# Kernel tuning notes

Measured on AMD Instinct MI355X. Metric: run time of the kernel, lower is better.

The kernel has to match this reference:

```python
import jax, jax.numpy as jnp
import numpy as np

EPS = 1.1920928955078125e-07  # torch fp32 default eps for F.rms_norm
N_HEADS = 16
HEAD_DIM = 128


def apply_rotary_emb(x, cos, sin):
    # x: [B,S,H,D]; cos/sin: [1,S,1,D/2]
    d = x.shape[-1] // 2
    x1, x2 = x[..., :d], x[..., d:]
    return jnp.concatenate([x1 * cos + x2 * sin, -x1 * sin + x2 * cos], axis=-1)


def rms_norm(x):
    # F.rms_norm over last dim, no learned weight
    ms = jnp.mean(jnp.square(x), axis=-1, keepdims=True)
    return x * jax.lax.rsqrt(ms + EPS)


def setup_inputs() -> dict:
    key = jax.random.key(0)
    ks = jax.random.split(key, 7)
    B, S, D = 2, 2048, 2048
    half = HEAD_DIM // 2
    # rotary tables (built like standard RoPE for realism)
    inv_freq = 1.0 / (10000.0 ** (np.arange(0, half, dtype=np.float32) / half))
    t = np.arange(S, dtype=np.float32)
    freqs = np.outer(t, inv_freq)  # [S, D/2]
    cos = jnp.asarray(np.cos(freqs))[None, :, None, :]
    sin = jnp.asarray(np.sin(freqs))[None, :, None, :]
    sd = 1.0 / np.sqrt(D)
    return {
        "x": jax.random.normal(ks[0], (B, S, D), jnp.float32),
        "cos": cos,
        "sin": sin,
        "Wq": jax.random.normal(ks[1], (D, D), jnp.float32) * sd,
        "Wk": jax.random.normal(ks[2], (D, D), jnp.float32) * sd,
        "Wv": jax.random.normal(ks[3], (D, D), jnp.float32) * sd,
        "Wo": jax.random.normal(ks[4], (D, D), jnp.float32) * sd,
    }


def reference(x, cos, sin, Wq, Wk, Wv, Wo):
    B, S, D = x.shape
    H, Hd = N_HEADS, HEAD_DIM
    q = (x @ Wq.T).reshape(B, S, H, Hd)
    k = (x @ Wk.T).reshape(B, S, H, Hd)
    v = (x @ Wv.T).reshape(B, S, H, Hd)
    q = apply_rotary_emb(q, cos[:, :S], sin[:, :S])
    k = apply_rotary_emb(k, cos[:, :S], sin[:, :S])
    q = rms_norm(q) * 1.2  # [B,S,H,Hd]
    k = rms_norm(k) * 1.2
    scale = 1.0 / jnp.sqrt(jnp.asarray(Hd, x.dtype))
    # scores: [B,H,Sq,Sk]
    scores = jnp.einsum("bqhd,bkhd->bhqk", q, k) * scale
    attn = jax.nn.softmax(scores, axis=-1)
    y = jnp.einsum("bhqk,bkhd->bqhd", attn, v).reshape(B, S, D)
    return y @ Wo.T
```

## Files before the change

### kernel.cpp

```cpp
#include <hip/hip_runtime.h>
#include <hip/hip_bf16.h>
#include <math.h>

typedef __bf16 bf16;
typedef __attribute__((ext_vector_type(8))) __bf16 bf16x8;
typedef __attribute__((ext_vector_type(4))) float f32x4;
typedef __attribute__((ext_vector_type(16))) float f32x16;

#define DEV __device__ __forceinline__

DEV void gload16(const void* g, void* l) {
    __builtin_amdgcn_global_load_lds(
        (__attribute__((address_space(1))) void*)(void*)g,
        (__attribute__((address_space(3))) void*)l, 16, 0, 0);
}

DEV unsigned pk2(float a, float b) {
    union { bf16 h[2]; unsigned u; } z;
    z.h[0] = (bf16)a; z.h[1] = (bf16)b;
    return z.u;
}

DEV void plswap(unsigned& a, unsigned& b) {
    asm volatile("v_permlane32_swap_b32 %0, %1" : "+v"(a), "+v"(b));
}

__global__ __launch_bounds__(256) void cvt_kernel(const float* __restrict__ in,
                                                  bf16* __restrict__ out, int n8) {
    for (int i = blockIdx.x * 256 + threadIdx.x; i < n8; i += gridDim.x * 256) {
        const float4* p = (const float4*)(in + (size_t)i * 8);
        float4 a = p[0], b = p[1];
        bf16x8 o;
        o[0] = (bf16)a.x; o[1] = (bf16)a.y; o[2] = (bf16)a.z; o[3] = (bf16)a.w;
        o[4] = (bf16)b.x; o[5] = (bf16)b.y; o[6] = (bf16)b.z; o[7] = (bf16)b.w;
        *(bf16x8*)(out + (size_t)i * 8) = o;
    }
}

template <bool F32OUT>
__global__ __launch_bounds__(256) void gemm_bt(const bf16* __restrict__ A,
                                               const bf16* __restrict__ B,
                                               void* __restrict__ Cout,
                                               int M, int N, int K) {
    __shared__ __align__(16) bf16 As[128 * 64];
    __shared__ __align__(16) bf16 Bs[128 * 64];
    const int tid = threadIdx.x, lane = tid & 63, wv = tid >> 6;
    const int tm = blockIdx.y * 128, tn = blockIdx.x * 128;
    const int wr = (wv >> 1) * 64, wc = (wv & 1) * 64;

    f32x4 acc[4][4] = {};
    const int scb = (lane & 7) * 16;

    for (int k0 = 0; k0 < K; k0 += 64) {
#pragma unroll
        for (int i = 0; i < 4; ++i) {
            int chunk = wv * 4 + i;
            int row = chunk * 8 + (lane >> 3);
            int cb = scb ^ ((row & 7) << 4);
            gload16((const char*)(A + (size_t)(tm + row) * K + k0) + cb,
                    (char*)As + chunk * 1024);
            gload16((const char*)(B + (size_t)(tn + row) * K + k0) + cb,
                    (char*)Bs + chunk * 1024);
        }
        __syncthreads();
#pragma unroll
        for (int kk = 0; kk < 2; ++kk) {
            bf16x8 af[4], bfr[4];
#pragma unroll
            for (int m = 0; m < 4; ++m) {
                int row = wr + m * 16 + (lane & 15);
                int cb = (kk * 64 + ((lane >> 4) * 16)) ^ ((row & 7) << 4);
                af[m] = *(const bf16x8*)((const char*)As + row * 128 + cb);
            }
#pragma unroll
            for (int n = 0; n < 4; ++n) {
                int row = wc + n * 16 + (lane & 15);
                int cb = (kk * 64 + ((lane >> 4) * 16)) ^ ((row & 7) << 4);
                bfr[n] = *(const bf16x8*)((const char*)Bs + row * 128 + cb);
            }
#pragma unroll
            for (int m = 0; m < 4; ++m)
#pragma unroll
                for (int n = 0; n < 4; ++n)
                    acc[m][n] = __builtin_amdgcn_mfma_f32_16x16x32_bf16(
                        af[m], bfr[n], acc[m][n], 0, 0, 0);
        }
        __syncthreads();
    }
#pragma unroll
    for (int m = 0; m < 4; ++m)
#pragma unroll
        for (int n = 0; n < 4; ++n)
#pragma unroll
            for (int r = 0; r < 4; ++r) {
                int row = tm + wr + m * 16 + (lane >> 4) * 4 + r;
                int col = tn + wc + n * 16 + (lane & 15);
                if (F32OUT)
                    ((float*)Cout)[(size_t)row * N + col] = acc[m][n][r];
                else
                    ((bf16*)Cout)[(size_t)row * N + col] = (bf16)acc[m][n][r];
            }
}

__global__ __launch_bounds__(256) void rope_rms(bf16* __restrict__ q,
                                                bf16* __restrict__ k,
                                                const float* __restrict__ cosp,
                                                const float* __restrict__ sinp) {
    int gw = blockIdx.x * 4 + (threadIdx.x >> 6);
    int lane = threadIdx.x & 63;
    bf16* base = (blockIdx.y == 0) ? q : k;
    int m = gw >> 4, h = gw & 15;
    int s = m & 2047;
    bf16* p = base + (size_t)m * 2048 + h * 128;
    float x1 = (float)p[lane], x2 = (float)p[lane + 64];
    float c = cosp[s * 64 + lane], si = sinp[s * 64 + lane];
    float r1 = x1 * c + x2 * si;
    float r2 = x2 * c - x1 * si;
    float ss = r1 * r1 + r2 * r2;
#pragma unroll
    for (int msk = 1; msk < 64; msk <<= 1) ss += __shfl_xor(ss, msk);
    float sc = rsqrtf(ss * (1.0f / 128.0f) + 1.1920928955078125e-07f) * 1.2f;
    if (blockIdx.y == 0) sc *= (0.08838834764831845f * 1.4426950408889634f);
    p[lane] = (bf16)(r1 * sc);
    p[lane + 64] = (bf16)(r2 * sc);
}

__global__ __launch_bounds__(256, 2) void attn_kernel(const bf16* __restrict__ q,
                                                      const bf16* __restrict__ k,
                                                      const bf16* __restrict__ v,
                                                      bf16* __restrict__ y) {
    __shared__ __align__(16) bf16 Ks[2][64 * 128];
    __shared__ __align__(16) bf16 Vt[2][128][72];

    const int tid = threadIdx.x, lane = tid & 63, wv = tid >> 6;
    const int q31 = lane & 31, h5 = lane >> 5;

    int wgid = blockIdx.y * 16 + blockIdx.x;
    int xcd = wgid & 7, j = wgid >> 3;
    int bh = xcd * 4 + (j >> 4);
    int qblk = j & 15;
    const int b = bh >> 4, h = bh & 15;
    const int q0 = qblk * 128;

    const bf16* qptr = q + (size_t)(b * 2048 + q0 + wv * 32 + q31) * 2048 +
                       h * 128 + h5 * 8;
    bf16x8 qf[8];
#pragma unroll
    for (int ks = 0; ks < 8; ++ks) qf[ks] = *(const bf16x8*)(qptr + ks * 16);

    float mrun = -INFINITY, lrun = 0.f;
    f32x16 acco[4] = {};

    const bf16* vbase = v + (size_t)(b * 2048 + wv * 16) * 2048 + h * 128 + 2 * lane;
    const bf16* kbase = k + (size_t)(b * 2048) * 2048 + h * 128;

    unsigned u[16];

    auto stageK = [&](int t, int buf) {
#pragma unroll
        for (int i = 0; i < 4; ++i) {
            int chunk = wv * 4 + i;
            int row = chunk * 4 + (lane >> 4);
            int cb = ((lane & 15) * 16) ^ ((row & 7) << 4);
            gload16((const char*)(kbase + (size_t)(t * 64 + row) * 2048) + cb,
                    (char*)(Ks[buf]) + chunk * 1024);
        }
    };
    auto loadV = [&](int t) {
        const bf16* vp = vbase + (size_t)(t * 64) * 2048;
#pragma unroll
        for (int jj = 0; jj < 16; ++jj)
            u[jj] = *(const unsigned*)(vp + (size_t)jj * 2048);
    };
    auto writeV = [&](int buf) {
        union { unsigned short s[8]; bf16x8 v8; } r0a, r0b, r1a, r1b;
#pragma unroll
        for (int jj = 0; jj < 8; ++jj) {
            r0a.s[jj] = (unsigned short)(u[jj] & 0xffff);
            r1a.s[jj] = (unsigned short)(u[jj] >> 16);
            r0b.s[jj] = (unsigned short)(u[jj + 8] & 0xffff);
            r1b.s[jj] = (unsigned short)(u[jj + 8] >> 16);
        }
        *(bf16x8*)(&Vt[buf][2 * lane][wv * 16]) = r0a.v8;
        *(bf16x8*)(&Vt[buf][2 * lane][wv * 16 + 8]) = r0b.v8;
        *(bf16x8*)(&Vt[buf][2 * lane + 1][wv * 16]) = r1a.v8;
        *(bf16x8*)(&Vt[buf][2 * lane + 1][wv * 16 + 8]) = r1b.v8;
    };

    stageK(0, 0);
    loadV(0);
    writeV(0);
    __syncthreads();

    for (int t = 0; t < 32; ++t) {
        const int c = t & 1;
        if (t < 31) {
            stageK(t + 1, c ^ 1);
            loadV(t + 1);
        }

        f32x16 st[2];
        __builtin_amdgcn_s_setprio(1);
#pragma unroll
        for (int kvb = 0; kvb < 2; ++kvb) {
            f32x16 a = {};
#pragma unroll
            for (int ks = 0; ks < 8; ++ks) {
                int row = kvb * 32 + q31;
                int cb = (32 * ks + 16 * h5) ^ ((row & 7) << 4);
                const bf16x8 kf =
                    *(const bf16x8*)((const char*)(Ks[c]) + row * 256 + cb);
                a = __builtin_amdgcn_mfma_f32_32x32x16_bf16(kf, qf[ks], a, 0, 0, 0);
            }
            st[kvb] = a;
        }
        __builtin_amdgcn_s_setprio(0);

        float t8[8];
#pragma unroll
        for (int r = 0; r < 8; ++r)
            t8[r] = fmaxf(fmaxf(st[0][r], st[0][r + 8]),
                          fmaxf(st[1][r], st[1][r + 8]));
        float mx = fmaxf(fmaxf(fmaxf(t8[0], t8[1]), fmaxf(t8[2], t8[3])),
                         fmaxf(fmaxf(t8[4], t8[5]), fmaxf(t8[6], t8[7])));
        mx = fmaxf(mx, __shfl_xor(mx, 32));

        if (__any(mx - mrun > 8.0f)) {
            float mn = fmaxf(mrun, mx);
            float alpha = exp2f(mrun - mn);
            mrun = mn;
            lrun *= alpha;
#pragma unroll
            for (int r = 0; r < 16; ++r) {
                int qr = (r & 3) + 8 * (r >> 2) + 4 * h5;
                float al = __shfl(alpha, qr);
                acco[0][r] *= al; acco[1][r] *= al;
                acco[2][r] *= al; acco[3][r] *= al;
            }
        }

        unsigned w[2][8];
        float rsa = 0.f, rsb = 0.f;
#pragma unroll
        for (int kvb = 0; kvb < 2; ++kvb)
#pragma unroll
            for (int i = 0; i < 8; ++i) {
                float p0 = exp2f(st[kvb][2 * i] - mrun);
                float p1 = exp2f(st[kvb][2 * i + 1] - mrun);
                if (i & 1) rsb += p0 + p1; else rsa += p0 + p1;
                w[kvb][i] = pk2(p0, p1);
            }
        float rs = rsa + rsb;
        rs += __shfl_xor(rs, 32);
        lrun += rs;

        __builtin_amdgcn_s_setprio(1);
#pragma unroll
        for (int b2 = 0; b2 < 2; ++b2)
#pragma unroll
            for (int ksl = 0; ksl < 2; ++ksl) {
                const int ks = b2 * 2 + ksl, u0 = ksl * 4;
                unsigned f0 = w[b2][u0 + 0], f2 = w[b2][u0 + 2];
                unsigned f1 = w[b2][u0 + 1], f3 = w[b2][u0 + 3];
                plswap(f0, f2);
                plswap(f1, f3);
                union { unsigned uu[4]; bf16x8 v8; } fr;
                fr.uu[0] = f0; fr.uu[1] = f1; fr.uu[2] = f2; fr.uu[3] = f3;
#pragma unroll
                for (int dblk = 0; dblk < 4; ++dblk) {
                    const bf16x8 vf = *(const bf16x8*)(
                        &Vt[c][dblk * 32 + q31][ks * 16 + h5 * 8]);
                    acco[dblk] = __builtin_amdgcn_mfma_f32_32x32x16_bf16(
                        fr.v8, vf, acco[dblk], 0, 0, 0);
                }
            }
        __builtin_amdgcn_s_setprio(0);

        if (t < 31) writeV(c ^ 1);
        __syncthreads();
    }

    float linv = 1.0f / lrun;
#pragma unroll
    for (int r = 0; r < 16; ++r) {
        int qr = (r & 3) + 8 * (r >> 2) + 4 * h5;
        float il = __shfl(linv, qr);
        size_t row = (size_t)(b * 2048 + q0 + wv * 32 + qr) * 2048 + h * 128;
#pragma unroll
        for (int dblk = 0; dblk < 4; ++dblk)
            y[row + dblk * 32 + q31] = (bf16)(acco[dblk][r] * il);
    }
}

extern "C" void kernel_launch(void* const* d_in, const int* in_sizes, int n_in,
                              void* d_out, int out_size, void* d_ws, size_t ws_size,
                              hipStream_t stream) {
    const float* x = (const float*)d_in[0];
    const float* cs = (const float*)d_in[1];
    const float* sn = (const float*)d_in[2];
    const float* Wq = (const float*)d_in[3];
    const float* Wk = (const float*)d_in[4];
    const float* Wv = (const float*)d_in[5];
    const float* Wo = (const float*)d_in[6];

    char* ws = (char*)d_ws;
    bf16* xb  = (bf16*)(ws + 0);
    bf16* wqb = (bf16*)(ws + 16777216);
    bf16* wkb = (bf16*)(ws + 25165824);
    bf16* wvb = (bf16*)(ws + 33554432);
    bf16* wob = (bf16*)(ws + 41943040);
    bf16* qb  = (bf16*)(ws + 50331648);
    bf16* kb  = (bf16*)(ws + 67108864);
    bf16* vb  = (bf16*)(ws + 83886080);
    bf16* yb  = (bf16*)(ws + 100663296);

    cvt_kernel<<<1024, 256, 0, stream>>>(x, xb, 8388608 / 8);
    cvt_kernel<<<512, 256, 0, stream>>>(Wq, wqb, 4194304 / 8);
    cvt_kernel<<<512, 256, 0, stream>>>(Wk, wkb, 4194304 / 8);
    cvt_kernel<<<512, 256, 0, stream>>>(Wv, wvb, 4194304 / 8);
    cvt_kernel<<<512, 256, 0, stream>>>(Wo, wob, 4194304 / 8);

    dim3 g(16, 32);
    gemm_bt<false><<<g, 256, 0, stream>>>(xb, wqb, qb, 4096, 2048, 2048);
    gemm_bt<false><<<g, 256, 0, stream>>>(xb, wkb, kb, 4096, 2048, 2048);
    gemm_bt<false><<<g, 256, 0, stream>>>(xb, wvb, vb, 4096, 2048, 2048);

    rope_rms<<<dim3(16384, 2), 256, 0, stream>>>(qb, kb, cs, sn);

    attn_kernel<<<dim3(16, 32), 256, 0, stream>>>(qb, kb, vb, yb);

    gemm_bt<true><<<g, 256, 0, stream>>>(yb, wob, d_out, 4096, 2048, 2048);
}
```

Measured before the change: 326.7 us.

## Double per-wave query rows in attention and merge weight conversion launches

Each attention wave now handles two 32-row query sub-tiles (256 queries per block), so every K and V fragment read from LDS feeds two MFMAs. This halves the grid to 256 blocks and lowers occupancy to one block per CU. The four weight fp32-to-bf16 conversions become a single launch. The changes aim to cut LDS traffic and K/V reloads per query and to save launch overhead, at the cost of higher register pressure and fewer resident waves to hide latency.

```diff
diff --git a/kernel.cpp b/kernel.cpp
--- a/kernel.cpp
+++ b/kernel.cpp
@@ -34,6 +34,24 @@
         o[0] = (bf16)a.x; o[1] = (bf16)a.y; o[2] = (bf16)a.z; o[3] = (bf16)a.w;
         o[4] = (bf16)b.x; o[5] = (bf16)b.y; o[6] = (bf16)b.z; o[7] = (bf16)b.w;
         *(bf16x8*)(out + (size_t)i * 8) = o;
+    }
+}
+
+__global__ __launch_bounds__(256) void cvtw_kernel(const float* __restrict__ w0,
+                                                   const float* __restrict__ w1,
+                                                   const float* __restrict__ w2,
+                                                   const float* __restrict__ w3,
+                                                   bf16* __restrict__ out) {
+    const float* in = (blockIdx.y == 0) ? w0 : (blockIdx.y == 1) ? w1
+                      : (blockIdx.y == 2) ? w2 : w3;
+    bf16* o = out + (size_t)blockIdx.y * 4194304;
+    for (int i = blockIdx.x * 256 + threadIdx.x; i < 524288; i += 512 * 256) {
+        const float4* p = (const float4*)(in + (size_t)i * 8);
+        float4 a = p[0], b = p[1];
+        bf16x8 v;
+        v[0] = (bf16)a.x; v[1] = (bf16)a.y; v[2] = (bf16)a.z; v[3] = (bf16)a.w;
+        v[4] = (bf16)b.x; v[5] = (bf16)b.y; v[6] = (bf16)b.z; v[7] = (bf16)b.w;
+        *(bf16x8*)(o + (size_t)i * 8) = v;
     }
 }
 
@@ -125,7 +143,7 @@
     p[lane + 64] = (bf16)(r2 * sc);
 }
 
-__global__ __launch_bounds__(256, 2) void attn_kernel(const bf16* __restrict__ q,
+__global__ __launch_bounds__(256, 1) void attn_kernel(const bf16* __restrict__ q,
                                                       const bf16* __restrict__ k,
                                                       const bf16* __restrict__ v,
                                                       bf16* __restrict__ y) {
@@ -135,21 +153,22 @@
     const int tid = threadIdx.x, lane = tid & 63, wv = tid >> 6;
     const int q31 = lane & 31, h5 = lane >> 5;
 
-    int wgid = blockIdx.y * 16 + blockIdx.x;
-    int xcd = wgid & 7, j = wgid >> 3;
-    int bh = xcd * 4 + (j >> 4);
-    int qblk = j & 15;
+    const int bh = blockIdx.x * 4 + (blockIdx.y >> 3);
+    const int qblk = blockIdx.y & 7;
     const int b = bh >> 4, h = bh & 15;
-    const int q0 = qblk * 128;
-
-    const bf16* qptr = q + (size_t)(b * 2048 + q0 + wv * 32 + q31) * 2048 +
-                       h * 128 + h5 * 8;
-    bf16x8 qf[8];
-#pragma unroll
-    for (int ks = 0; ks < 8; ++ks) qf[ks] = *(const bf16x8*)(qptr + ks * 16);
-
-    float mrun = -INFINITY, lrun = 0.f;
-    f32x16 acco[4] = {};
+    const int q0 = qblk * 256;
+
+    bf16x8 qf[2][8];
+#pragma unroll
+    for (int qh = 0; qh < 2; ++qh) {
+        const bf16* qptr = q + (size_t)(b * 2048 + q0 + wv * 64 + qh * 32 + q31) * 2048 +
+                           h * 128 + h5 * 8;
+#pragma unroll
+        for (int ks = 0; ks < 8; ++ks) qf[qh][ks] = *(const bf16x8*)(qptr + ks * 16);
+    }
+
+    float mrun[2] = {-INFINITY, -INFINITY}, lrun[2] = {0.f, 0.f};
+    f32x16 acco[2][4] = {};
 
     const bf16* vbase = v + (size_t)(b * 2048 + wv * 16) * 2048 + h * 128 + 2 * lane;
     const bf16* kbase = k + (size_t)(b * 2048) * 2048 + h * 128;
@@ -199,60 +218,63 @@
             loadV(t + 1);
         }
 
-        f32x16 st[2];
+        f32x16 st[2][2] = {};
         __builtin_amdgcn_s_setprio(1);
 #pragma unroll
-        for (int kvb = 0; kvb < 2; ++kvb) {
-            f32x16 a = {};
+        for (int kvb = 0; kvb < 2; ++kvb)
 #pragma unroll
             for (int ks = 0; ks < 8; ++ks) {
                 int row = kvb * 32 + q31;
                 int cb = (32 * ks + 16 * h5) ^ ((row & 7) << 4);
                 const bf16x8 kf =
                     *(const bf16x8*)((const char*)(Ks[c]) + row * 256 + cb);
-                a = __builtin_amdgcn_mfma_f32_32x32x16_bf16(kf, qf[ks], a, 0, 0, 0);
-            }
-            st[kvb] = a;
-        }
+                st[0][kvb] = __builtin_amdgcn_mfma_f32_32x32x16_bf16(
+                    kf, qf[0][ks], st[0][kvb], 0, 0, 0);
+                st[1][kvb] = __builtin_amdgcn_mfma_f32_32x32x16_bf16(
+                    kf, qf[1][ks], st[1][kvb], 0, 0, 0);
+            }
         __builtin_amdgcn_s_setprio(0);
 
-        float t8[8];
-#pragma unroll
-        for (int r = 0; r < 8; ++r)
-            t8[r] = fmaxf(fmaxf(st[0][r], st[0][r + 8]),
-                          fmaxf(st[1][r], st[1][r + 8]));
-        float mx = fmaxf(fmaxf(fmaxf(t8[0], t8[1]), fmaxf(t8[2], t8[3])),
-                         fmaxf(fmaxf(t8[4], t8[5]), fmaxf(t8[6], t8[7])));
-        mx = fmaxf(mx, __shfl_xor(mx, 32));
-
-        if (__any(mx - mrun > 8.0f)) {
-            float mn = fmaxf(mrun, mx);
-            float alpha = exp2f(mrun - mn);
-            mrun = mn;
-            lrun *= alpha;
-#pragma unroll
-            for (int r = 0; r < 16; ++r) {
-                int qr = (r & 3) + 8 * (r >> 2) + 4 * h5;
-                float al = __shfl(alpha, qr);
-                acco[0][r] *= al; acco[1][r] *= al;
-                acco[2][r] *= al; acco[3][r] *= al;
-            }
-        }
-
-        unsigned w[2][8];
-        float rsa = 0.f, rsb = 0.f;
-#pragma unroll
-        for (int kvb = 0; kvb < 2; ++kvb)
-#pragma unroll
-            for (int i = 0; i < 8; ++i) {
-                float p0 = exp2f(st[kvb][2 * i] - mrun);
-                float p1 = exp2f(st[kvb][2 * i + 1] - mrun);
-                if (i & 1) rsb += p0 + p1; else rsa += p0 + p1;
-                w[kvb][i] = pk2(p0, p1);
-            }
-        float rs = rsa + rsb;
-        rs += __shfl_xor(rs, 32);
-        lrun += rs;
+        unsigned w[2][2][8];
+#pragma unroll
+        for (int qh = 0; qh < 2; ++qh) {
+            float t8[8];
+#pragma unroll
+            for (int r = 0; r < 8; ++r)
+                t8[r] = fmaxf(fmaxf(st[qh][0][r], st[qh][0][r + 8]),
+                              fmaxf(st[qh][1][r], st[qh][1][r + 8]));
+            float mx = fmaxf(fmaxf(fmaxf(t8[0], t8[1]), fmaxf(t8[2], t8[3])),
+                             fmaxf(fmaxf(t8[4], t8[5]), fmaxf(t8[6], t8[7])));
+            mx = fmaxf(mx, __shfl_xor(mx, 32));
+
+            if (__any(mx - mrun[qh] > 8.0f)) {
+                float mn = fmaxf(mrun[qh], mx);
+                float alpha = exp2f(mrun[qh] - mn);
+                mrun[qh] = mn;
+                lrun[qh] *= alpha;
+#pragma unroll
+                for (int r = 0; r < 16; ++r) {
+                    int qr = (r & 3) + 8 * (r >> 2) + 4 * h5;
+                    float al = __shfl(alpha, qr);
+                    acco[qh][0][r] *= al; acco[qh][1][r] *= al;
+                    acco[qh][2][r] *= al; acco[qh][3][r] *= al;
+                }
+            }
+
+            float rsa = 0.f, rsb = 0.f;
+#pragma unroll
+            for (int kvb = 0; kvb < 2; ++kvb)
+#pragma unroll
+                for (int i = 0; i < 8; ++i) {
+                    float p0 = exp2f(st[qh][kvb][2 * i] - mrun[qh]);
+                    float p1 = exp2f(st[qh][kvb][2 * i + 1] - mrun[qh]);
+                    if (i & 1) rsb += p0 + p1; else rsa += p0 + p1;
+                    w[qh][kvb][i] = pk2(p0, p1);
+                }
+            float rs = rsa + rsb;
+            rs += __shfl_xor(rs, 32);
+            lrun[qh] += rs;
+        }
 
         __builtin_amdgcn_s_setprio(1);
 #pragma unroll
@@ -260,18 +282,24 @@
 #pragma unroll
             for (int ksl = 0; ksl < 2; ++ksl) {
                 const int ks = b2 * 2 + ksl, u0 = ksl * 4;
-                unsigned f0 = w[b2][u0 + 0], f2 = w[b2][u0 + 2];
-                unsigned f1 = w[b2][u0 + 1], f3 = w[b2][u0 + 3];
-                plswap(f0, f2);
-                plswap(f1, f3);
-                union { unsigned uu[4]; bf16x8 v8; } fr;
-                fr.uu[0] = f0; fr.uu[1] = f1; fr.uu[2] = f2; fr.uu[3] = f3;
+                union { unsigned uu[4]; bf16x8 v8; } fr[2];
+#pragma unroll
+                for (int qh = 0; qh < 2; ++qh) {
+                    unsigned f0 = w[qh][b2][u0 + 0], f2 = w[qh][b2][u0 + 2];
+                    unsigned f1 = w[qh][b2][u0 + 1], f3 = w[qh][b2][u0 + 3];
+                    plswap(f0, f2);
+                    plswap(f1, f3);
+                    fr[qh].uu[0] = f0; fr[qh].uu[1] = f1;
+                    fr[qh].uu[2] = f2; fr[qh].uu[3] = f3;
+                }
 #pragma unroll
                 for (int dblk = 0; dblk < 4; ++dblk) {
                     const bf16x8 vf = *(const bf16x8*)(
                         &Vt[c][dblk * 32 + q31][ks * 16 + h5 * 8]);
-                    acco[dblk] = __builtin_amdgcn_mfma_f32_32x32x16_bf16(
-                        fr.v8, vf, acco[dblk], 0, 0, 0);
+                    acco[0][dblk] = __builtin_amdgcn_mfma_f32_32x32x16_bf16(
+                        fr[0].v8, vf, acco[0][dblk], 0, 0, 0);
+                    acco[1][dblk] = __builtin_amdgcn_mfma_f32_32x32x16_bf16(
+                        fr[1].v8, vf, acco[1][dblk], 0, 0, 0);
                 }
             }
         __builtin_amdgcn_s_setprio(0);
@@ -280,15 +308,19 @@
         __syncthreads();
     }
 
-    float linv = 1.0f / lrun;
-#pragma unroll
-    for (int r = 0; r < 16; ++r) {
-        int qr = (r & 3) + 8 * (r >> 2) + 4 * h5;
-        float il = __shfl(linv, qr);
-        size_t row = (size_t)(b * 2048 + q0 + wv * 32 + qr) * 2048 + h * 128;
-#pragma unroll
-        for (int dblk = 0; dblk < 4; ++dblk)
-            y[row + dblk * 32 + q31] = (bf16)(acco[dblk][r] * il);
+#pragma unroll
+    for (int qh = 0; qh < 2; ++qh) {
+        float linv = 1.0f / lrun[qh];
+#pragma unroll
+        for (int r = 0; r < 16; ++r) {
+            int qr = (r & 3) + 8 * (r >> 2) + 4 * h5;
+            float il = __shfl(linv, qr);
+            size_t row = (size_t)(b * 2048 + q0 + wv * 64 + qh * 32 + qr) * 2048 +
+                         h * 128;
+#pragma unroll
+            for (int dblk = 0; dblk < 4; ++dblk)
+                y[row + dblk * 32 + q31] = (bf16)(acco[qh][dblk][r] * il);
+        }
     }
 }
 
@@ -315,10 +347,7 @@
     bf16* yb  = (bf16*)(ws + 100663296);
 
     cvt_kernel<<<1024, 256, 0, stream>>>(x, xb, 8388608 / 8);
-    cvt_kernel<<<512, 256, 0, stream>>>(Wq, wqb, 4194304 / 8);
-    cvt_kernel<<<512, 256, 0, stream>>>(Wk, wkb, 4194304 / 8);
-    cvt_kernel<<<512, 256, 0, stream>>>(Wv, wvb, 4194304 / 8);
-    cvt_kernel<<<512, 256, 0, stream>>>(Wo, wob, 4194304 / 8);
+    cvtw_kernel<<<dim3(512, 4), 256, 0, stream>>>(Wq, Wk, Wv, Wo, wqb);
 
     dim3 g(16, 32);
     gemm_bt<false><<<g, 256, 0, stream>>>(xb, wqb, qb, 4096, 2048, 2048);
@@ -327,7 +356,7 @@
 
     rope_rms<<<dim3(16384, 2), 256, 0, stream>>>(qb, kb, cs, sn);
 
-    attn_kernel<<<dim3(16, 32), 256, 0, stream>>>(qb, kb, vb, yb);
+    attn_kernel<<<dim3(8, 32), 256, 0, stream>>>(qb, kb, vb, yb);
 
     gemm_bt<true><<<g, 256, 0, stream>>>(yb, wob, d_out, 4096, 2048, 2048);
 }
```

Measured after the change: 353.6 us. 8.2% more time.

## Fuse QKV projections into one double-buffered 256x256 GEMM and batch weight casts

Applied to the files above, without the earlier changes.

Replaces the three separate Q/K/V projection GEMMs with a single GEMM over the concatenated weight matrix. It uses 256x256 tiles, 512 threads, double-buffered LDS with swizzled layout, phased MFMA scheduling with priority hints, and a tile-order swizzle for L2 locality. The four weight conversions are merged into one launch writing contiguous bf16 weights. This cuts launch count and raises per-tile data reuse, but relies on the workspace layout placing wq/wk/wv contiguously and uses more LDS and registers per block.

```diff
diff --git a/kernel.cpp b/kernel.cpp
--- a/kernel.cpp
+++ b/kernel.cpp
@@ -35,6 +35,161 @@
         o[4] = (bf16)b.x; o[5] = (bf16)b.y; o[6] = (bf16)b.z; o[7] = (bf16)b.w;
         *(bf16x8*)(out + (size_t)i * 8) = o;
     }
+}
+
+__global__ __launch_bounds__(256) void cvtw_kernel(const float* __restrict__ w0,
+                                                   const float* __restrict__ w1,
+                                                   const float* __restrict__ w2,
+                                                   const float* __restrict__ w3,
+                                                   bf16* __restrict__ out) {
+    const float* in = (blockIdx.y == 0) ? w0 : (blockIdx.y == 1) ? w1
+                      : (blockIdx.y == 2) ? w2 : w3;
+    bf16* o = out + (size_t)blockIdx.y * 4194304;
+    for (int i = blockIdx.x * 256 + threadIdx.x; i < 524288; i += 512 * 256) {
+        const float4* p = (const float4*)(in + (size_t)i * 8);
+        float4 a = p[0], b = p[1];
+        bf16x8 v;
+        v[0] = (bf16)a.x; v[1] = (bf16)a.y; v[2] = (bf16)a.z; v[3] = (bf16)a.w;
+        v[4] = (bf16)b.x; v[5] = (bf16)b.y; v[6] = (bf16)b.z; v[7] = (bf16)b.w;
+        *(bf16x8*)(o + (size_t)i * 8) = v;
+    }
+}
+
+__global__ __launch_bounds__(512, 2) void gemm_qkv(const bf16* __restrict__ A,
+                                                   const bf16* __restrict__ Bg,
+                                                   bf16* __restrict__ outq,
+                                                   int M, int K) {
+    __shared__ __align__(16) bf16 As[2][256 * 64];
+    __shared__ __align__(16) bf16 Bs[2][256 * 64];
+    const int tid = threadIdx.x, lane = tid & 63, wv = tid >> 6;
+    const int ql = lane & 15, hi = lane >> 4;
+    const int wm = wv >> 2, wn = wv & 3;
+
+    int lin = blockIdx.y * 24 + blockIdx.x;
+    int swz = (lin & 7) * 48 + (lin >> 3);
+    const int tm = (swz / 24) * 256;
+    const int tn = (swz % 24) * 256;
+
+    bf16* outp = outq + (size_t)(tn >> 11) * 8388608 + (tn & 2047);
+
+    f32x4 acc[8][4] = {};
+
+    auto stage = [&](int t, int buf) {
+#pragma unroll
+        for (int i = 0; i < 4; ++i) {
+            int chunk = wv * 4 + i;
+            int row = chunk * 8 + (lane >> 3);
+            int cb = ((lane & 7) * 16) ^ ((row & 7) << 4);
+            gload16((const char*)(A + (size_t)(tm + row) * K + t * 64) + cb,
+                    (char*)(As[buf]) + chunk * 1024);
+            gload16((const char*)(Bg + (size_t)(tn + row) * K + t * 64) + cb,
+                    (char*)(Bs[buf]) + chunk * 1024);
+        }
+    };
+    auto rdA = [&](int buf, int mf, int ks) -> bf16x8 {
+        int row = wm * 128 + mf * 16 + ql;
+        int cb = (ks * 64 + hi * 16) ^ ((row & 7) << 4);
+        return *(const bf16x8*)((const char*)(As[buf]) + row * 128 + cb);
+    };
+    auto rdB = [&](int buf, int nf, int ks) -> bf16x8 {
+        int row = wn * 64 + nf * 16 + ql;
+        int cb = (ks * 64 + hi * 16) ^ ((row & 7) << 4);
+        return *(const bf16x8*)((const char*)(Bs[buf]) + row * 128 + cb);
+    };
+
+    stage(0, 0);
+    __syncthreads();
+
+    for (int t = 0; t < 32; ++t) {
+        const int c = t & 1;
+        bf16x8 af[4][2], bfr[2][2];
+#pragma unroll
+        for (int mf = 0; mf < 4; ++mf)
+#pragma unroll
+            for (int ks = 0; ks < 2; ++ks) af[mf][ks] = rdA(c, mf, ks);
+#pragma unroll
+        for (int nf = 0; nf < 2; ++nf)
+#pragma unroll
+            for (int ks = 0; ks < 2; ++ks) bfr[nf][ks] = rdB(c, nf, ks);
+        if (t < 31) stage(t + 1, c ^ 1);
+        asm volatile("s_waitcnt lgkmcnt(8)" ::: "memory");
+        __builtin_amdgcn_s_barrier();
+        asm volatile("s_waitcnt lgkmcnt(0)" ::: "memory");
+        __builtin_amdgcn_sched_barrier(0);
+        __builtin_amdgcn_s_setprio(1);
+#pragma unroll
+        for (int mf = 0; mf < 4; ++mf)
+#pragma unroll
+            for (int nf = 0; nf < 2; ++nf)
+#pragma unroll
+                for (int ks = 0; ks < 2; ++ks)
+                    acc[mf][nf] = __builtin_amdgcn_mfma_f32_16x16x32_bf16(
+                        af[mf][ks], bfr[nf][ks], acc[mf][nf], 0, 0, 0);
+        __builtin_amdgcn_s_setprio(0);
+        __builtin_amdgcn_s_barrier();
+#pragma unroll
+        for (int nf = 0; nf < 2; ++nf)
+#pragma unroll
+            for (int ks = 0; ks < 2; ++ks) bfr[nf][ks] = rdB(c, 2 + nf, ks);
+        __builtin_amdgcn_s_barrier();
+        asm volatile("s_waitcnt lgkmcnt(0)" ::: "memory");
+        __builtin_amdgcn_sched_barrier(0);
+        __builtin_amdgcn_s_setprio(1);
+#pragma unroll
+        for (int mf = 0; mf < 4; ++mf)
+#pragma unroll
+            for (int nf = 0; nf < 2; ++nf)
+#pragma unroll
+                for (int ks = 0; ks < 2; ++ks)
+                    acc[mf][2 + nf] = __builtin_amdgcn_mfma_f32_16x16x32_bf16(
+                        af[mf][ks], bfr[nf][ks], acc[mf][2 + nf], 0, 0, 0);
+        __builtin_amdgcn_s_setprio(0);
+        __builtin_amdgcn_s_barrier();
+#pragma unroll
+        for (int mf = 0; mf < 4; ++mf)
+#pragma unroll
+            for (int ks = 0; ks < 2; ++ks) af[mf][ks] = rdA(c, 4 + mf, ks);
+        __builtin_amdgcn_s_barrier();
+        asm volatile("s_waitcnt lgkmcnt(0)" ::: "memory");
+        __builtin_amdgcn_sched_barrier(0);
+        __builtin_amdgcn_s_setprio(1);
+#pragma unroll
+        for (int mf = 0; mf < 4; ++mf)
+#pragma unroll
+            for (int nf = 0; nf < 2; ++nf)
+#pragma unroll
+                for (int ks = 0; ks < 2; ++ks)
+                    acc[4 + mf][2 + nf] = __builtin_amdgcn_mfma_f32_16x16x32_bf16(
+                        af[mf][ks], bfr[nf][ks], acc[4 + mf][2 + nf], 0, 0, 0);
+        __builtin_amdgcn_s_setprio(0);
+        __builtin_amdgcn_s_barrier();
+#pragma unroll
+        for (int nf = 0; nf < 2; ++nf)
+#pragma unroll
+            for (int ks = 0; ks < 2; ++ks) bfr[nf][ks] = rdB(c, nf, ks);
+        __syncthreads();
+        __builtin_amdgcn_s_setprio(1);
+#pragma unroll
+        for (int mf = 0; mf < 4; ++mf)
+#pragma unroll
+            for (int nf = 0; nf < 2; ++nf)
+#pragma unroll
+                for (int ks = 0; ks < 2; ++ks)
+                    acc[4 + mf][nf] = __builtin_amdgcn_mfma_f32_16x16x32_bf16(
+                        af[mf][ks], bfr[nf][ks], acc[4 + mf][nf], 0, 0, 0);
+        __builtin_amdgcn_s_setprio(0);
+    }
+
+#pragma unroll
+    for (int mf = 0; mf < 8; ++mf)
+#pragma unroll
+        for (int nf = 0; nf < 4; ++nf)
+#pragma unroll
+            for (int r = 0; r < 4; ++r) {
+                int row = tm + wm * 128 + mf * 16 + hi * 4 + r;
+                int col = wn * 64 + nf * 16 + ql;
+                outp[(size_t)row * 2048 + col] = (bf16)acc[mf][nf][r];
+            }
 }
 
 template <bool F32OUT>
@@ -306,8 +461,6 @@
     char* ws = (char*)d_ws;
     bf16* xb  = (bf16*)(ws + 0);
     bf16* wqb = (bf16*)(ws + 16777216);
-    bf16* wkb = (bf16*)(ws + 25165824);
-    bf16* wvb = (bf16*)(ws + 33554432);
     bf16* wob = (bf16*)(ws + 41943040);
     bf16* qb  = (bf16*)(ws + 50331648);
     bf16* kb  = (bf16*)(ws + 67108864);
@@ -315,19 +468,14 @@
     bf16* yb  = (bf16*)(ws + 100663296);
 
     cvt_kernel<<<1024, 256, 0, stream>>>(x, xb, 8388608 / 8);
-    cvt_kernel<<<512, 256, 0, stream>>>(Wq, wqb, 4194304 / 8);
-    cvt_kernel<<<512, 256, 0, stream>>>(Wk, wkb, 4194304 / 8);
-    cvt_kernel<<<512, 256, 0, stream>>>(Wv, wvb, 4194304 / 8);
-    cvt_kernel<<<512, 256, 0, stream>>>(Wo, wob, 4194304 / 8);
+    cvtw_kernel<<<dim3(512, 4), 256, 0, stream>>>(Wq, Wk, Wv, Wo, wqb);
+
+    gemm_qkv<<<dim3(24, 16), 512, 0, stream>>>(xb, wqb, qb, 4096, 2048);
+
+    rope_rms<<<dim3(16384, 2), 256, 0, stream>>>(qb, kb, cs, sn);
+
+    attn_kernel<<<dim3(16, 32), 256, 0, stream>>>(qb, kb, vb, yb);
 
     dim3 g(16, 32);
-    gemm_bt<false><<<g, 256, 0, stream>>>(xb, wqb, qb, 4096, 2048, 2048);
-    gemm_bt<false><<<g, 256, 0, stream>>>(xb, wkb, kb, 4096, 2048, 2048);
-    gemm_bt<false><<<g, 256, 0, stream>>>(xb, wvb, vb, 4096, 2048, 2048);
-
-    rope_rms<<<dim3(16384, 2), 256, 0, stream>>>(qb, kb, cs, sn);
-
-    attn_kernel<<<dim3(16, 32), 256, 0, stream>>>(qb, kb, vb, yb);
-
     gemm_bt<true><<<g, 256, 0, stream>>>(yb, wob, d_out, 4096, 2048, 2048);
 }
```

Result: faster. 313.7 us (-4.0%).

## Fuse QKV projections into one triple-buffered 32x32 MFMA GEMM and batch weight casts

Applied to the files above, without the earlier changes.

The three separate Q/K/V projection GEMMs are replaced by one GEMM over the concatenated weight matrix (N=6144). It uses 256x384 tiles, 512 threads, 32x32x16 bf16 MFMA, a three-stage global_load_lds pipeline with XOR-swizzled LDS, and a tile-order swizzle. The four weight conversion launches are merged into one kernel that writes the weights contiguously, which the fused GEMM relies on. This aims to cut launch count and reuse x tiles across all three projections, at the cost of large LDS use and scattered 2-byte stores in the epilogue.

```diff
diff --git a/kernel.cpp b/kernel.cpp
--- a/kernel.cpp
+++ b/kernel.cpp
@@ -23,6 +23,10 @@
 
 DEV void plswap(unsigned& a, unsigned& b) {
     asm volatile("v_permlane32_swap_b32 %0, %1" : "+v"(a), "+v"(b));
+}
+
+DEV f32x16 mfma32(bf16x8 a, bf16x8 b, f32x16 c) {
+    return __builtin_amdgcn_mfma_f32_32x32x16_bf16(a, b, c, 0, 0, 0);
 }
 
 __global__ __launch_bounds__(256) void cvt_kernel(const float* __restrict__ in,
@@ -35,6 +39,143 @@
         o[4] = (bf16)b.x; o[5] = (bf16)b.y; o[6] = (bf16)b.z; o[7] = (bf16)b.w;
         *(bf16x8*)(out + (size_t)i * 8) = o;
     }
+}
+
+__global__ __launch_bounds__(256) void cvtw_kernel(const float* __restrict__ w0,
+                                                   const float* __restrict__ w1,
+                                                   const float* __restrict__ w2,
+                                                   const float* __restrict__ w3,
+                                                   bf16* __restrict__ out) {
+    const float* in = (blockIdx.y == 0) ? w0 : (blockIdx.y == 1) ? w1
+                      : (blockIdx.y == 2) ? w2 : w3;
+    bf16* o = out + (size_t)blockIdx.y * 4194304;
+    for (int i = blockIdx.x * 256 + threadIdx.x; i < 524288; i += 512 * 256) {
+        const float4* p = (const float4*)(in + (size_t)i * 8);
+        float4 a = p[0], b = p[1];
+        bf16x8 v;
+        v[0] = (bf16)a.x; v[1] = (bf16)a.y; v[2] = (bf16)a.z; v[3] = (bf16)a.w;
+        v[4] = (bf16)b.x; v[5] = (bf16)b.y; v[6] = (bf16)b.z; v[7] = (bf16)b.w;
+        *(bf16x8*)(o + (size_t)i * 8) = v;
+    }
+}
+
+__global__ __launch_bounds__(512, 2) void gemm_qkv(const bf16* __restrict__ A,
+                                                   const bf16* __restrict__ Bg,
+                                                   bf16* __restrict__ outq) {
+    __shared__ __align__(16) bf16 As[3][256 * 32];
+    __shared__ __align__(16) bf16 Bs[3][384 * 32];
+    const int tid = threadIdx.x, lane = tid & 63, wv = tid >> 6;
+    const int q31 = lane & 31, h5 = lane >> 5;
+    const int wm = wv >> 2, wn = wv & 3;
+    const int K = 2048;
+
+    int lin = blockIdx.x;
+    int swz = (lin & 7) * 32 + (lin >> 3);
+    const int tm = (swz >> 4) * 256;
+    const int tn = (swz & 15) * 384;
+
+    f32x16 acc[4][3] = {};
+
+    auto stageA = [&](int t, int buf) {
+#pragma unroll
+        for (int l = 0; l < 2; ++l) {
+            int chunk = l * 8 + wv;
+            int row = chunk * 16 + (lane >> 2);
+            int cb = ((lane & 3) * 16) ^ ((row & 3) << 4);
+            gload16((const char*)(A + (size_t)(tm + row) * K + t * 32) + cb,
+                    (char*)(As[buf]) + chunk * 1024);
+        }
+    };
+    auto stageB = [&](int t, int buf) {
+#pragma unroll
+        for (int l = 0; l < 3; ++l) {
+            int chunk = l * 8 + wv;
+            int row = chunk * 16 + (lane >> 2);
+            int cb = ((lane & 3) * 16) ^ ((row & 3) << 4);
+            gload16((const char*)(Bg + (size_t)(tn + row) * K + t * 32) + cb,
+                    (char*)(Bs[buf]) + chunk * 1024);
+        }
+    };
+    auto rdA = [&](int buf, int mb, int ks) -> bf16x8 {
+        int row = wm * 128 + mb * 32 + q31;
+        int off = (ks * 32 + h5 * 16) ^ ((row & 3) << 4);
+        return *(const bf16x8*)((const char*)(As[buf]) + row * 64 + off);
+    };
+    auto rdB = [&](int buf, int nb, int ks) -> bf16x8 {
+        int row = wn * 96 + nb * 32 + q31;
+        int off = (ks * 32 + h5 * 16) ^ ((row & 3) << 4);
+        return *(const bf16x8*)((const char*)(Bs[buf]) + row * 64 + off);
+    };
+
+    stageA(0, 0); stageB(0, 0);
+    stageA(1, 1); stageB(1, 1);
+    asm volatile("s_waitcnt vmcnt(5)" ::: "memory");
+    __builtin_amdgcn_s_barrier();
+
+    int cur = 0, nxt2 = 2;
+    for (int t = 0; t < 64; ++t) {
+        bf16x8 af[2][2], bfr[3][2];
+#pragma unroll
+        for (int mb = 0; mb < 2; ++mb)
+#pragma unroll
+            for (int ks = 0; ks < 2; ++ks) af[mb][ks] = rdA(cur, mb, ks);
+#pragma unroll
+        for (int nb = 0; nb < 3; ++nb)
+#pragma unroll
+            for (int ks = 0; ks < 2; ++ks) bfr[nb][ks] = rdB(cur, nb, ks);
+        if (t < 62) stageA(t + 2, nxt2);
+        __builtin_amdgcn_s_barrier();
+        asm volatile("s_waitcnt lgkmcnt(0)" ::: "memory");
+        __builtin_amdgcn_sched_barrier(0);
+        __builtin_amdgcn_s_setprio(1);
+#pragma unroll
+        for (int mb = 0; mb < 2; ++mb)
+#pragma unroll
+            for (int nb = 0; nb < 3; ++nb)
+#pragma unroll
+                for (int ks = 0; ks < 2; ++ks)
+                    acc[mb][nb] = mfma32(af[mb][ks], bfr[nb][ks], acc[mb][nb]);
+        __builtin_amdgcn_s_setprio(0);
+        __builtin_amdgcn_s_barrier();
+#pragma unroll
+        for (int mb = 0; mb < 2; ++mb)
+#pragma unroll
+            for (int ks = 0; ks < 2; ++ks) af[mb][ks] = rdA(cur, 2 + mb, ks);
+        if (t < 62) stageB(t + 2, nxt2);
+        __builtin_amdgcn_s_barrier();
+        asm volatile("s_waitcnt lgkmcnt(0)" ::: "memory");
+        __builtin_amdgcn_sched_barrier(0);
+        __builtin_amdgcn_s_setprio(1);
+#pragma unroll
+        for (int mb = 0; mb < 2; ++mb)
+#pragma unroll
+            for (int nb = 0; nb < 3; ++nb)
+#pragma unroll
+                for (int ks = 0; ks < 2; ++ks)
+                    acc[2 + mb][nb] = mfma32(af[mb][ks], bfr[nb][ks], acc[2 + mb][nb]);
+        __builtin_amdgcn_s_setprio(0);
+        if (t < 62)
+            asm volatile("s_waitcnt vmcnt(5)" ::: "memory");
+        else
+            asm volatile("s_waitcnt vmcnt(0)" ::: "memory");
+        __builtin_amdgcn_s_barrier();
+        cur = (cur == 2) ? 0 : cur + 1;
+        nxt2 = (nxt2 == 2) ? 0 : nxt2 + 1;
+    }
+
+#pragma unroll
+    for (int mb = 0; mb < 4; ++mb)
+#pragma unroll
+        for (int nb = 0; nb < 3; ++nb) {
+            int colbase = tn + wn * 96 + nb * 32;
+            bf16* op = outq + (size_t)(colbase >> 11) * 8388608 +
+                       (colbase & 2047) + q31;
+#pragma unroll
+            for (int r = 0; r < 16; ++r) {
+                int row = tm + wm * 128 + mb * 32 + (r & 3) + 8 * (r >> 2) + 4 * h5;
+                op[(size_t)row * 2048] = (bf16)acc[mb][nb][r];
+            }
+        }
 }
 
 template <bool F32OUT>
@@ -306,8 +447,6 @@
     char* ws = (char*)d_ws;
     bf16* xb  = (bf16*)(ws + 0);
     bf16* wqb = (bf16*)(ws + 16777216);
-    bf16* wkb = (bf16*)(ws + 25165824);
-    bf16* wvb = (bf16*)(ws + 33554432);
     bf16* wob = (bf16*)(ws + 41943040);
     bf16* qb  = (bf16*)(ws + 50331648);
     bf16* kb  = (bf16*)(ws + 67108864);
@@ -315,19 +454,14 @@
     bf16* yb  = (bf16*)(ws + 100663296);
 
     cvt_kernel<<<1024, 256, 0, stream>>>(x, xb, 8388608 / 8);
-    cvt_kernel<<<512, 256, 0, stream>>>(Wq, wqb, 4194304 / 8);
-    cvt_kernel<<<512, 256, 0, stream>>>(Wk, wkb, 4194304 / 8);
-    cvt_kernel<<<512, 256, 0, stream>>>(Wv, wvb, 4194304 / 8);
-    cvt_kernel<<<512, 256, 0, stream>>>(Wo, wob, 4194304 / 8);
+    cvtw_kernel<<<dim3(512, 4), 256, 0, stream>>>(Wq, Wk, Wv, Wo, wqb);
+
+    gemm_qkv<<<256, 512, 0, stream>>>(xb, wqb, qb);
+
+    rope_rms<<<dim3(16384, 2), 256, 0, stream>>>(qb, kb, cs, sn);
+
+    attn_kernel<<<dim3(16, 32), 256, 0, stream>>>(qb, kb, vb, yb);
 
     dim3 g(16, 32);
-    gemm_bt<false><<<g, 256, 0, stream>>>(xb, wqb, qb, 4096, 2048, 2048);
-    gemm_bt<false><<<g, 256, 0, stream>>>(xb, wkb, kb, 4096, 2048, 2048);
-    gemm_bt<false><<<g, 256, 0, stream>>>(xb, wvb, vb, 4096, 2048, 2048);
-
-    rope_rms<<<dim3(16384, 2), 256, 0, stream>>>(qb, kb, cs, sn);
-
-    attn_kernel<<<dim3(16, 32), 256, 0, stream>>>(qb, kb, vb, yb);
-
     gemm_bt<true><<<g, 256, 0, stream>>>(yb, wob, d_out, 4096, 2048, 2048);
 }
```

New measurement: 297.8 us. 8.8% less time.
